# Performance work log

Hardware: AMD Instinct MI355X
Metric: run time of the kernel (lower is better)

## Reference

```python
import jax, jax.numpy as jnp
import numpy as np


def setup_inputs() -> dict:
    key = jax.random.key(0)
    ks = jax.random.split(key, 8)
    B, T, U, D, H, V = 4, 128, 64, 512, 640, 1024
    return {
        "source_encodings": jax.random.normal(ks[0], (B, T, D), dtype=jnp.float32),
        "source_lengths": jax.random.randint(ks[1], (B,), 1, T + 1).astype(jnp.int32),
        "target_encodings": jax.random.normal(ks[2], (B, U, D), dtype=jnp.float32),
        "target_lengths": jax.random.randint(ks[3], (B,), 1, U + 1).astype(jnp.int32),
        "W1": jax.random.normal(ks[4], (2 * D, H), dtype=jnp.float32) * (1.0 / np.sqrt(2 * D)),
        "b1": jax.random.normal(ks[5], (H,), dtype=jnp.float32) * 0.01,
        "W2": jax.random.normal(ks[6], (H, V), dtype=jnp.float32) * (1.0 / np.sqrt(H)),
        "b2": jax.random.normal(ks[7], (V,), dtype=jnp.float32) * 0.01,
    }


def reference(source_encodings, source_lengths, target_encodings, target_lengths, W1, b1, W2, b2):
    # CONCAT combination: Linear(concat(s, t)) == s @ W1[:D] + t @ W1[D:] + b1.
    # This avoids materializing the [B,T,U,2D] expand+concat tensor while
    # computing identical math to the original torch module.
    D = source_encodings.shape[-1]
    W1s, W1t = W1[:D], W1[D:]
    ps = jnp.einsum("btd,dh->bth", source_encodings, W1s)   # [B,T,H]
    pt = jnp.einsum("bud,dh->buh", target_encodings, W1t)   # [B,U,H]
    h = jnp.tanh(ps[:, :, None, :] + pt[:, None, :, :] + b1)  # [B,T,U,H]
    logits = jnp.einsum("btuh,hv->btuv", h, W2) + b2          # [B,T,U,V]
    # Module is in eval mode (not self.training) -> log_softmax applied.
    out = jax.nn.log_softmax(logits, axis=-1)
    return (out, source_lengths, target_lengths)
```

## Files before the change

### kernel.cpp

```cpp
#include <hip/hip_runtime.h>
#include <hip/hip_bf16.h>

#define B_ 4
#define T_ 128
#define U_ 64
#define D_ 512
#define H_ 640
#define V_ 1024

typedef float f32x4 __attribute__((ext_vector_type(4)));
typedef __bf16 bf16x8 __attribute__((ext_vector_type(8)));

union U4BF8 { uint4 u; bf16x8 v; };

__device__ __forceinline__ unsigned short f2bf(float x) {
  union { float f; unsigned int u; } a; a.f = x;
  unsigned int r = a.u + 0x7FFFu + ((a.u >> 16) & 1u);
  return (unsigned short)(r >> 16);
}

__global__ void k_pack_w2(const float* __restrict__ W2, uint4* __restrict__ w2p,
                          const int* __restrict__ slen, const int* __restrict__ tlen,
                          float* __restrict__ out_tail) {
  int kq = blockIdx.x;
  int tid = threadIdx.x;
  for (int i = 0; i < 4; ++i) {
    int n = tid + i * 256;
    int src_n = (n & ~63) | ((n & 15) * 4) | ((n >> 4) & 3);
    float f[8];
    #pragma unroll
    for (int j = 0; j < 8; ++j) f[j] = W2[(size_t)(kq * 8 + j) * V_ + src_n];
    unsigned int w[4];
    #pragma unroll
    for (int j = 0; j < 4; ++j)
      w[j] = (unsigned)f2bf(f[2 * j]) | ((unsigned)f2bf(f[2 * j + 1]) << 16);
    uint4 p; p.x = w[0]; p.y = w[1]; p.z = w[2]; p.w = w[3];
    w2p[(size_t)kq * V_ + n] = p;
  }
  if (blockIdx.x == 0 && tid < 8)
    out_tail[tid] = (tid < 4) ? (float)slen[tid] : (float)tlen[tid - 4];
}

__global__ __launch_bounds__(640) void k_proj(
    const float* __restrict__ src, const float* __restrict__ tgt,
    const float* __restrict__ W1, const float* __restrict__ b1,
    float* __restrict__ ps, float* __restrict__ pt) {
  __shared__ __align__(16) float lin[D_ * 4];
  int bid = blockIdx.x, tid = threadIdx.x;
  bool is_t = bid >= 128;
  const float* in; const float* w; float* outp;
  if (!is_t) {
    int r0 = bid * 4;
    in = src + (size_t)r0 * D_; w = W1; outp = ps + (size_t)r0 * H_;
  } else {
    int r0 = (bid - 128) * 4;
    in = tgt + (size_t)r0 * D_; w = W1 + (size_t)D_ * H_; outp = pt + (size_t)r0 * H_;
  }
  for (int idx = tid; idx < 4 * D_; idx += 640) {
    int r = idx >> 9, k = idx & (D_ - 1);
    lin[k * 4 + r] = in[idx];
  }
  __syncthreads();
  float a0 = 0.f, a1 = 0.f, a2 = 0.f, a3 = 0.f;
  int j = tid;
  for (int k = 0; k < D_; ++k) {
    float wv = w[(size_t)k * H_ + j];
    f32x4 x = *(const f32x4*)&lin[k * 4];
    a0 += x[0] * wv; a1 += x[1] * wv; a2 += x[2] * wv; a3 += x[3] * wv;
  }
  float bb = is_t ? b1[j] : 0.f;
  outp[0 * H_ + j] = a0 + bb;
  outp[1 * H_ + j] = a1 + bb;
  outp[2 * H_ + j] = a2 + bb;
  outp[3 * H_ + j] = a3 + bb;
}

__global__ __launch_bounds__(1024, 4) void k_joint(
    const float* __restrict__ ps, const float* __restrict__ pt,
    const uint4* __restrict__ w2p, const float* __restrict__ b2,
    float* __restrict__ out) {
  __shared__ uint4 ldsA[80 * 64];
  __shared__ float red[16][64][2];
  __shared__ float lzs[64];
  int bid = blockIdx.x;
  int xcd = bid & 7;
  int b = xcd >> 1;
  int t = (bid >> 3) + (xcd & 1) * 64;
  int tid = threadIdx.x;
  int lane = tid & 63, wid = tid >> 6;
  int l16 = lane & 15, lg = lane >> 4;
  int xs = l16 & 7;
  const float* psrow = ps + (size_t)(b * T_ + t) * H_;
  const float* ptb   = pt + (size_t)(b * U_) * H_;

  for (int c = tid; c < 80 * 64; c += 1024) {
    int m = c / 80, kq = c - m * 80;
    const float4* pp = (const float4*)(psrow + kq * 8);
    const float4* qq = (const float4*)(ptb + (size_t)m * H_ + kq * 8);
    float4 p0 = pp[0], p1 = pp[1];
    float4 q0 = qq[0], q1 = qq[1];
    float x[8] = {p0.x + q0.x, p0.y + q0.y, p0.z + q0.z, p0.w + q0.w,
                  p1.x + q1.x, p1.y + q1.y, p1.z + q1.z, p1.w + q1.w};
    unsigned int wv[4];
    #pragma unroll
    for (int j = 0; j < 4; ++j) {
      float e0 = __expf(2.f * x[2 * j]);
      float h0 = 1.f - 2.f * __builtin_amdgcn_rcpf(e0 + 1.f);
      float e1 = __expf(2.f * x[2 * j + 1]);
      float h1 = 1.f - 2.f * __builtin_amdgcn_rcpf(e1 + 1.f);
      wv[j] = (unsigned)f2bf(h0) | ((unsigned)f2bf(h1) << 16);
    }
    uint4 pk; pk.x = wv[0]; pk.y = wv[1]; pk.z = wv[2]; pk.w = wv[3];
    ldsA[m * 80 + (kq ^ (m & 7))] = pk;
  }
  __syncthreads();

  f32x4 acc[4][4];
  #pragma unroll
  for (int mf = 0; mf < 4; ++mf)
    #pragma unroll
    for (int nf = 0; nf < 4; ++nf) {
      f32x4 z = {0.f, 0.f, 0.f, 0.f};
      acc[mf][nf] = z;
    }

  for (int kq0 = 0; kq0 < 80; kq0 += 4) {
    int kq = kq0 + lg;
    U4BF8 a[4];
    #pragma unroll
    for (int mf = 0; mf < 4; ++mf)
      a[mf].u = ldsA[(mf * 16 + l16) * 80 + (kq ^ xs)];
    const uint4* bp = w2p + (size_t)kq * 1024 + wid * 64 + l16;
    #pragma unroll
    for (int nf = 0; nf < 4; ++nf) {
      U4BF8 bb; bb.u = bp[nf * 16];
      #pragma unroll
      for (int mf = 0; mf < 4; ++mf)
        acc[mf][nf] = __builtin_amdgcn_mfma_f32_16x16x32_bf16(
            a[mf].v, bb.v, acc[mf][nf], 0, 0, 0);
    }
  }

  {
    f32x4 b2v = *(const f32x4*)&b2[wid * 64 + l16 * 4];
    #pragma unroll
    for (int mf = 0; mf < 4; ++mf)
      #pragma unroll
      for (int nf = 0; nf < 4; ++nf)
        #pragma unroll
        for (int r = 0; r < 4; ++r)
          acc[mf][nf][r] += b2v[nf];
  }

  #pragma unroll
  for (int mf = 0; mf < 4; ++mf)
    #pragma unroll
    for (int r = 0; r < 4; ++r) {
      float pm = -3.4e38f;
      #pragma unroll
      for (int nf = 0; nf < 4; ++nf) pm = fmaxf(pm, acc[mf][nf][r]);
      pm = fmaxf(pm, __shfl_xor(pm, 1));
      pm = fmaxf(pm, __shfl_xor(pm, 2));
      pm = fmaxf(pm, __shfl_xor(pm, 4));
      pm = fmaxf(pm, __shfl_xor(pm, 8));
      float s = 0.f;
      #pragma unroll
      for (int nf = 0; nf < 4; ++nf) s += __expf(acc[mf][nf][r] - pm);
      s += __shfl_xor(s, 1);
      s += __shfl_xor(s, 2);
      s += __shfl_xor(s, 4);
      s += __shfl_xor(s, 8);
      if (l16 == 0) {
        int row = mf * 16 + lg * 4 + r;
        red[wid][row][0] = pm;
        red[wid][row][1] = s;
      }
    }
  __syncthreads();

  if (tid < 64) {
    float M = -3.4e38f;
    #pragma unroll
    for (int w16 = 0; w16 < 16; ++w16) M = fmaxf(M, red[w16][tid][0]);
    float S = 0.f;
    #pragma unroll
    for (int w16 = 0; w16 < 16; ++w16)
      S += red[w16][tid][1] * __expf(red[w16][tid][0] - M);
    lzs[tid] = M + __logf(S);
  }
  __syncthreads();

  float* outb = out + (size_t)(b * T_ + t) * U_ * V_;
  #pragma unroll
  for (int mf = 0; mf < 4; ++mf)
    #pragma unroll
    for (int r = 0; r < 4; ++r) {
      int row = mf * 16 + lg * 4 + r;
      float lz = lzs[row];
      f32x4 o;
      o[0] = acc[mf][0][r] - lz;
      o[1] = acc[mf][1][r] - lz;
      o[2] = acc[mf][2][r] - lz;
      o[3] = acc[mf][3][r] - lz;
      __builtin_nontemporal_store(
          o, (f32x4*)&outb[(size_t)row * V_ + wid * 64 + l16 * 4]);
    }
}

extern "C" void kernel_launch(void* const* d_in, const int* in_sizes, int n_in,
                              void* d_out, int out_size, void* d_ws, size_t ws_size,
                              hipStream_t stream) {
  const float* src = (const float*)d_in[0];
  const int*   slen = (const int*)d_in[1];
  const float* tgt = (const float*)d_in[2];
  const int*   tlen = (const int*)d_in[3];
  const float* W1 = (const float*)d_in[4];
  const float* b1 = (const float*)d_in[5];
  const float* W2 = (const float*)d_in[6];
  const float* b2 = (const float*)d_in[7];
  float* out = (float*)d_out;

  float* ps  = (float*)d_ws;
  float* pt  = ps + 512 * 640;
  uint4* w2p = (uint4*)(pt + 256 * 640);

  k_pack_w2<<<80, 256, 0, stream>>>(W2, w2p, slen, tlen,
                                    out + (size_t)B_ * T_ * U_ * V_);
  k_proj<<<192, 640, 0, stream>>>(src, tgt, W1, b1, ps, pt);
  k_joint<<<512, 1024, 0, stream>>>(ps, pt, w2p, b2, out);
}
```

Before: 112.9 us.

## Double-buffer tanh A-tile generation in chunks to overlap with MFMA

The joint kernel no longer builds the whole 64x640 bf16 tanh tile in LDS before the GEMM. It now produces K-chunks of 16 (x8) into a two-slot LDS buffer, generating the next chunk while MFMAs run on the current one. This shrinks LDS use from 80KB to 32KB, which could allow more resident blocks, and hides the tanh and global-load latency behind compute. The cost is a __syncthreads per chunk and more live registers during the loop.

```diff
diff --git a/kernel.cpp b/kernel.cpp
--- a/kernel.cpp
+++ b/kernel.cpp
@@ -79,7 +79,7 @@
     const float* __restrict__ ps, const float* __restrict__ pt,
     const uint4* __restrict__ w2p, const float* __restrict__ b2,
     float* __restrict__ out) {
-  __shared__ uint4 ldsA[80 * 64];
+  __shared__ uint4 ldsA[2][64 * 16];
   __shared__ float red[16][64][2];
   __shared__ float lzs[64];
   int bid = blockIdx.x;
@@ -90,30 +90,11 @@
   int lane = tid & 63, wid = tid >> 6;
   int l16 = lane & 15, lg = lane >> 4;
   int xs = l16 & 7;
+  int gm = tid >> 4;
+  int gk = tid & 15;
+  int gcell = gm * 16 + (gk ^ (gm & 7));
   const float* psrow = ps + (size_t)(b * T_ + t) * H_;
-  const float* ptb   = pt + (size_t)(b * U_) * H_;
-
-  for (int c = tid; c < 80 * 64; c += 1024) {
-    int m = c / 80, kq = c - m * 80;
-    const float4* pp = (const float4*)(psrow + kq * 8);
-    const float4* qq = (const float4*)(ptb + (size_t)m * H_ + kq * 8);
-    float4 p0 = pp[0], p1 = pp[1];
-    float4 q0 = qq[0], q1 = qq[1];
-    float x[8] = {p0.x + q0.x, p0.y + q0.y, p0.z + q0.z, p0.w + q0.w,
-                  p1.x + q1.x, p1.y + q1.y, p1.z + q1.z, p1.w + q1.w};
-    unsigned int wv[4];
-    #pragma unroll
-    for (int j = 0; j < 4; ++j) {
-      float e0 = __expf(2.f * x[2 * j]);
-      float h0 = 1.f - 2.f * __builtin_amdgcn_rcpf(e0 + 1.f);
-      float e1 = __expf(2.f * x[2 * j + 1]);
-      float h1 = 1.f - 2.f * __builtin_amdgcn_rcpf(e1 + 1.f);
-      wv[j] = (unsigned)f2bf(h0) | ((unsigned)f2bf(h1) << 16);
-    }
-    uint4 pk; pk.x = wv[0]; pk.y = wv[1]; pk.z = wv[2]; pk.w = wv[3];
-    ldsA[m * 80 + (kq ^ (m & 7))] = pk;
-  }
-  __syncthreads();
+  const float* ptrow = pt + (size_t)(b * U_ + gm) * H_;
 
   f32x4 acc[4][4];
   #pragma unroll
@@ -124,22 +105,53 @@
       acc[mf][nf] = z;
     }
 
-  for (int kq0 = 0; kq0 < 80; kq0 += 4) {
-    int kq = kq0 + lg;
-    U4BF8 a[4];
-    #pragma unroll
-    for (int mf = 0; mf < 4; ++mf)
-      a[mf].u = ldsA[(mf * 16 + l16) * 80 + (kq ^ xs)];
-    const uint4* bp = w2p + (size_t)kq * 1024 + wid * 64 + l16;
-    #pragma unroll
-    for (int nf = 0; nf < 4; ++nf) {
-      U4BF8 bb; bb.u = bp[nf * 16];
+#define GEN_CHUNK(CK, BUF)                                                    \
+  {                                                                           \
+    int kq = (CK) * 16 + gk;                                                  \
+    const float4* pp = (const float4*)(psrow + kq * 8);                       \
+    const float4* qq = (const float4*)(ptrow + kq * 8);                       \
+    float4 p0 = pp[0], p1 = pp[1];                                            \
+    float4 q0 = qq[0], q1 = qq[1];                                            \
+    float x[8] = {p0.x + q0.x, p0.y + q0.y, p0.z + q0.z, p0.w + q0.w,         \
+                  p1.x + q1.x, p1.y + q1.y, p1.z + q1.z, p1.w + q1.w};        \
+    unsigned int wv[4];                                                       \
+    _Pragma("unroll")                                                         \
+    for (int j = 0; j < 4; ++j) {                                             \
+      float e0 = __expf(2.f * x[2 * j]);                                      \
+      float h0 = 1.f - 2.f * __builtin_amdgcn_rcpf(e0 + 1.f);                 \
+      float e1 = __expf(2.f * x[2 * j + 1]);                                  \
+      float h1 = 1.f - 2.f * __builtin_amdgcn_rcpf(e1 + 1.f);                 \
+      wv[j] = (unsigned)f2bf(h0) | ((unsigned)f2bf(h1) << 16);                \
+    }                                                                         \
+    uint4 pk; pk.x = wv[0]; pk.y = wv[1]; pk.z = wv[2]; pk.w = wv[3];         \
+    ldsA[BUF][gcell] = pk;                                                    \
+  }
+
+  GEN_CHUNK(0, 0);
+
+  for (int ck = 0; ck < 5; ++ck) {
+    __syncthreads();
+    if (ck < 4) GEN_CHUNK(ck + 1, (ck + 1) & 1);
+    const uint4* bufA = ldsA[ck & 1];
+    #pragma unroll
+    for (int kq0 = 0; kq0 < 16; kq0 += 4) {
+      int kql = kq0 + lg;
+      U4BF8 a[4];
       #pragma unroll
       for (int mf = 0; mf < 4; ++mf)
-        acc[mf][nf] = __builtin_amdgcn_mfma_f32_16x16x32_bf16(
-            a[mf].v, bb.v, acc[mf][nf], 0, 0, 0);
-    }
-  }
+        a[mf].u = bufA[(mf * 16 + l16) * 16 + (kql ^ xs)];
+      const uint4* bp = w2p + (size_t)(ck * 16 + kql) * 1024 + wid * 64 + l16;
+      #pragma unroll
+      for (int nf = 0; nf < 4; ++nf) {
+        U4BF8 bb; bb.u = bp[nf * 16];
+        #pragma unroll
+        for (int mf = 0; mf < 4; ++mf)
+          acc[mf][nf] = __builtin_amdgcn_mfma_f32_16x16x32_bf16(
+              a[mf].v, bb.v, acc[mf][nf], 0, 0, 0);
+      }
+    }
+  }
+#undef GEN_CHUNK
 
   {
     f32x4 b2v = *(const f32x4*)&b2[wid * 64 + l16 * 4];
```

Result: slower. 123.3 us (+9.2%).
